# Kernel tuning notes

Measured on AMD Instinct MI355X. Metric: run time of the kernel, lower is better.

Reference implementation:

```python
import jax, jax.numpy as jnp
import numpy as np

RADIUS = 50.0
EPS = 1e-8


def setup_inputs() -> dict:
    key = jax.random.key(0)
    k1, k2, k3, k4, k5 = jax.random.split(key, 5)
    N, E, H = 16384, 524288, 256
    x = jax.random.normal(k1, (N, H), dtype=jnp.float32)
    edge_index = jax.random.randint(k2, (2, E), 0, N, dtype=jnp.int32)
    spatial_coords = jax.random.uniform(k3, (N, 2), dtype=jnp.float32) * 1000.0
    w1 = jax.random.normal(k4, (3, H // 2), dtype=jnp.float32) * 0.02
    b1 = jnp.zeros((H // 2,), dtype=jnp.float32)
    w2 = jax.random.normal(k5, (H // 2, H), dtype=jnp.float32) * 0.02
    b2 = jnp.zeros((H,), dtype=jnp.float32)
    return {"x": x, "edge_index": edge_index, "spatial_coords": spatial_coords,
            "w1": w1, "b1": b1, "w2": w2, "b2": b2}


def reference(x, edge_index, spatial_coords, w1, b1, w2, b2):
    N = x.shape[0]
    row, col = edge_index[0], edge_index[1]

    # degree via scatter-add (segment_sum)
    ones = jnp.ones(row.shape, dtype=x.dtype)
    degree = jax.ops.segment_sum(ones, row, num_segments=N)  # [N]

    # spatial density: count neighbors within RADIUS (full pairwise, vectorized)
    sq = jnp.sum(spatial_coords * spatial_coords, axis=-1)  # [N]
    d2 = sq[:, None] + sq[None, :] - 2.0 * (spatial_coords @ spatial_coords.T)  # [N,N] squared dists
    in_radius = (d2 <= RADIUS * RADIUS).astype(x.dtype)
    density = jnp.sum(in_radius, axis=1) - 1.0  # exclude self
    density = density / (jnp.max(density) + EPS)

    # local feature variance: || x - mean(neighbor features) ||
    nbr_sum = jax.ops.segment_sum(x[col], row, num_segments=N)  # [N,H]
    cnt = jnp.clip(degree, 1.0)[:, None]
    nbr_mean = nbr_sum / cnt
    fvar = jnp.linalg.norm(x - nbr_mean, axis=-1)  # [N]
    fvar = fvar / (jnp.max(fvar) + EPS)

    feats = jnp.stack([degree / (jnp.max(degree) + EPS), density, fvar], axis=-1)  # [N,3]
    h = jax.nn.relu(feats @ w1 + b1)
    return h @ w2 + b2  # [N, hidden_dim]
```

## Files before the change

### kernel.cpp

```cpp
#include <hip/hip_runtime.h>
#include <math.h>

#define R2 2500.0f
#define EPSF 1e-8f

constexpr int H  = 256;
constexpr int HH = 128;

__global__ void k_degree(const int* __restrict__ row, int* __restrict__ deg, int E) {
    int e = blockIdx.x * blockDim.x + threadIdx.x;
    if (e < E) atomicAdd(&deg[row[e]], 1);
}

__global__ void k_scan(const int* __restrict__ deg, int* __restrict__ row_ptr, int N) {
    __shared__ int s[1024];
    int t = threadIdx.x;
    int per = N >> 10;
    int base = t * per;
    int vals[32];
    int local = 0;
    for (int k = 0; k < per; k++) { vals[k] = deg[base + k]; local += vals[k]; }
    s[t] = local;
    __syncthreads();
    for (int off = 1; off < 1024; off <<= 1) {
        int v = s[t];
        int add = (t >= off) ? s[t - off] : 0;
        __syncthreads();
        s[t] = v + add;
        __syncthreads();
    }
    int excl = (t > 0) ? s[t - 1] : 0;
    for (int k = 0; k < per; k++) { row_ptr[base + k] = excl; excl += vals[k]; }
    if (t == 1023) row_ptr[N] = excl;
}

__global__ void k_fill(const int* __restrict__ row, const int* __restrict__ col,
                       const int* __restrict__ row_ptr, int* __restrict__ fill,
                       int* __restrict__ cols, int E) {
    int e = blockIdx.x * blockDim.x + threadIdx.x;
    if (e < E) {
        int r = row[e];
        int p = row_ptr[r] + atomicAdd(&fill[r], 1);
        cols[p] = col[e];
    }
}

__global__ void k_density(const float* __restrict__ coords, int* __restrict__ dens,
                          int N, int jPer) {
    __shared__ float sx[256], sy[256], sq[256];
    int i = blockIdx.x * 256 + threadIdx.x;
    const float2* c2 = (const float2*)coords;
    float2 ci = c2[i];
    float sqi = ci.x * ci.x + ci.y * ci.y;
    int j0 = blockIdx.y * jPer;
    int cnt = 0;
    for (int jt = j0; jt < j0 + jPer; jt += 256) {
        float2 cj = c2[jt + threadIdx.x];
        sx[threadIdx.x] = cj.x;
        sy[threadIdx.x] = cj.y;
        sq[threadIdx.x] = cj.x * cj.x + cj.y * cj.y;
        __syncthreads();
#pragma unroll 8
        for (int k = 0; k < 256; k++) {
            float dot = ci.x * sx[k] + ci.y * sy[k];
            float d2 = (sqi + sq[k]) - 2.0f * dot;
            cnt += (d2 <= R2) ? 1 : 0;
        }
        __syncthreads();
    }
    atomicAdd(&dens[i], cnt);
}

__global__ void __launch_bounds__(256) k_fvar(
    const float* __restrict__ x, const int* __restrict__ row_ptr,
    const int* __restrict__ cols, float* __restrict__ fvar, int N) {
    __shared__ float4 lds[4][8][64];
    int wave = threadIdx.x >> 6;
    int lane = threadIdx.x & 63;
    int i = blockIdx.x * 4 + wave;
    int s = row_ptr[i], e = row_ptr[i + 1];
    const float4* xb = (const float4*)x;
    float4 acc = make_float4(0.f, 0.f, 0.f, 0.f);
    for (int p0 = s; p0 < e; p0 += 64) {
        int m = e - p0; if (m > 64) m = 64;
        int idx = cols[p0 + (lane < m ? lane : m - 1)];
        for (int j = 0; j < m; j += 8) {
            int nb = m - j; if (nb > 8) nb = 8;
#pragma unroll
            for (int k = 0; k < 8; k++) {
                if (k < nb) {
                    int c = __shfl(idx, j + k, 64);
                    const float4* gp = xb + (size_t)c * 64 + lane;
                    __builtin_amdgcn_global_load_lds(
                        (const __attribute__((address_space(1))) void*)gp,
                        (__attribute__((address_space(3))) void*)(&lds[wave][k][0]),
                        16, 0, 0);
                }
            }
            __builtin_amdgcn_s_waitcnt(0);
#pragma unroll
            for (int k = 0; k < 8; k++) {
                if (k < nb) {
                    float4 v = lds[wave][k][lane];
                    acc.x += v.x; acc.y += v.y; acc.z += v.z; acc.w += v.w;
                }
            }
        }
    }
    float cnt = fmaxf((float)(e - s), 1.0f);
    float4 xi = xb[(size_t)i * 64 + lane];
    float dx = xi.x - acc.x / cnt;
    float dy = xi.y - acc.y / cnt;
    float dz = xi.z - acc.z / cnt;
    float dw = xi.w - acc.w / cnt;
    float ss = dx * dx + dy * dy + dz * dz + dw * dw;
#pragma unroll
    for (int off = 32; off > 0; off >>= 1) ss += __shfl_xor(ss, off, 64);
    if (lane == 0) fvar[i] = sqrtf(ss);
}

__global__ void __launch_bounds__(256) k_scal(
    const int* __restrict__ deg, const int* __restrict__ dens,
    const float* __restrict__ fvar, int* __restrict__ scal, int N) {
    __shared__ int sd[4], sn[4];
    __shared__ float sf[4];
    int t = threadIdx.x;
    int g = blockIdx.x * 256 + t;
    int stride = 256 * gridDim.x;
    int md = 0, mn = 0;
    float mf = 0.f;
    for (int i = g; i < N; i += stride) {
        md = max(md, deg[i]);
        mn = max(mn, dens[i]);
        mf = fmaxf(mf, fvar[i]);
    }
#pragma unroll
    for (int off = 32; off > 0; off >>= 1) {
        md = max(md, __shfl_xor(md, off, 64));
        mn = max(mn, __shfl_xor(mn, off, 64));
        mf = fmaxf(mf, __shfl_xor(mf, off, 64));
    }
    int w = t >> 6, l = t & 63;
    if (l == 0) { sd[w] = md; sn[w] = mn; sf[w] = mf; }
    __syncthreads();
    if (t == 0) {
#pragma unroll
        for (int k = 1; k < 4; k++) {
            md = max(md, sd[k]);
            mn = max(mn, sn[k]);
            mf = fmaxf(mf, sf[k]);
        }
        atomicMax(&scal[0], md);
        atomicMax(&scal[1], mn);
        atomicMax(&scal[2], __float_as_int(mf));
    }
}

__global__ void __launch_bounds__(256) k_mlp(
    const float* __restrict__ w1, const float* __restrict__ b1,
    const float* __restrict__ w2, const float* __restrict__ b2,
    const int* __restrict__ deg, const int* __restrict__ dens,
    const float* __restrict__ fvar, const int* __restrict__ scal,
    float* __restrict__ out, int N) {
    __shared__ float sh_h[HH];
    int j = threadIdx.x;
    float wv[HH];
#pragma unroll
    for (int l = 0; l < HH; l++) wv[l] = w2[l * H + j];
    float bj = b2[j];
    float maxdeg  = (float)scal[0] + EPSF;
    float maxdens = (float)(scal[1] - 1) + EPSF;
    float maxfv   = __int_as_float(scal[2]) + EPSF;
    float w1a = 0.f, w1b = 0.f, w1c = 0.f, b1j = 0.f;
    if (j < HH) { w1a = w1[j]; w1b = w1[HH + j]; w1c = w1[2 * HH + j]; b1j = b1[j]; }
    for (int i = blockIdx.x; i < N; i += gridDim.x) {
        float f0 = (float)deg[i] / maxdeg;
        float f1 = (float)(dens[i] - 1) / maxdens;
        float f2 = fvar[i] / maxfv;
        if (j < HH) {
            float h = f0 * w1a + f1 * w1b + f2 * w1c + b1j;
            sh_h[j] = fmaxf(h, 0.0f);
        }
        __syncthreads();
        float acc = bj;
#pragma unroll
        for (int l = 0; l < HH; l++) acc = fmaf(sh_h[l], wv[l], acc);
        out[(size_t)i * H + j] = acc;
        __syncthreads();
    }
}

extern "C" void kernel_launch(void* const* d_in, const int* in_sizes, int n_in,
                              void* d_out, int out_size, void* d_ws, size_t ws_size,
                              hipStream_t stream) {
    const float* x      = (const float*)d_in[0];
    const int*   ei     = (const int*)d_in[1];
    const float* coords = (const float*)d_in[2];
    const float* w1     = (const float*)d_in[3];
    const float* b1     = (const float*)d_in[4];
    const float* w2     = (const float*)d_in[5];
    const float* b2     = (const float*)d_in[6];
    float* out = (float*)d_out;

    const int N = in_sizes[2] / 2;
    const int E = in_sizes[1] / 2;
    const int* row = ei;
    const int* col = ei + E;

    int* ws       = (int*)d_ws;
    int* deg_cnt  = ws;
    int* dens_cnt = ws + N;
    int* fill     = ws + 2 * N;
    int* scal     = ws + 3 * N;
    float* fvarp  = (float*)(ws + 3 * N + 4);
    int* row_ptr  = ws + 4 * N + 4;
    int* cols     = ws + 5 * N + 5;

    hipMemsetAsync(ws, 0, (size_t)(3 * N + 4) * sizeof(int), stream);

    int eb = (E + 255) / 256;
    k_degree<<<eb, 256, 0, stream>>>(row, deg_cnt, E);
    k_scan<<<1, 1024, 0, stream>>>(deg_cnt, row_ptr, N);
    k_fill<<<eb, 256, 0, stream>>>(row, col, row_ptr, fill, cols, E);

    const int NSLICE = 8;
    k_density<<<dim3(N / 256, NSLICE), 256, 0, stream>>>(coords, dens_cnt, N, N / NSLICE);

    k_fvar<<<N / 4, 256, 0, stream>>>(x, row_ptr, cols, fvarp, N);

    k_scal<<<64, 256, 0, stream>>>(deg_cnt, dens_cnt, fvarp, scal, N);

    k_mlp<<<1024, 256, 0, stream>>>(w1, b1, w2, b2, deg_cnt, dens_cnt, fvarp, scal,
                                    out, N);
}
```

Baseline: 297.4 us.

## Double-buffer neighbor gather in fvar and precompute packed coords for density

The fvar kernel now double-buffers its LDS gather: the next batch of eight neighbor rows is issued before the current batch is consumed, using a partial vmcnt wait so loads overlap accumulation. Its blocks shrink to two waves. A new prep kernel packs x, y and squared norm into a float4 per point, so the density kernel reads uniform global float4 loads in place of staging through shared memory with barriers. The density j-range is also split into 16 slices instead of 8. The risks are the hand-written waitcnt logic, clamped duplicate loads for partial batches, and an extra kernel launch.

```diff
diff --git a/kernel.cpp b/kernel.cpp
--- a/kernel.cpp
+++ b/kernel.cpp
@@ -45,63 +45,74 @@
     }
 }
 
-__global__ void k_density(const float* __restrict__ coords, int* __restrict__ dens,
-                          int N, int jPer) {
-    __shared__ float sx[256], sy[256], sq[256];
+__global__ void k_prep(const float* __restrict__ coords, float4* __restrict__ pj, int N) {
+    int i = blockIdx.x * 256 + threadIdx.x;
+    if (i < N) {
+        float2 c = ((const float2*)coords)[i];
+        pj[i] = make_float4(c.x, c.y, c.x * c.x + c.y * c.y, 0.0f);
+    }
+}
+
+__global__ void __launch_bounds__(256) k_density(
+    const float* __restrict__ coords, const float4* __restrict__ pj,
+    int* __restrict__ dens, int N, int jPer) {
     int i = blockIdx.x * 256 + threadIdx.x;
     const float2* c2 = (const float2*)coords;
     float2 ci = c2[i];
     float sqi = ci.x * ci.x + ci.y * ci.y;
     int j0 = blockIdx.y * jPer;
     int cnt = 0;
-    for (int jt = j0; jt < j0 + jPer; jt += 256) {
-        float2 cj = c2[jt + threadIdx.x];
-        sx[threadIdx.x] = cj.x;
-        sy[threadIdx.x] = cj.y;
-        sq[threadIdx.x] = cj.x * cj.x + cj.y * cj.y;
-        __syncthreads();
 #pragma unroll 8
-        for (int k = 0; k < 256; k++) {
-            float dot = ci.x * sx[k] + ci.y * sy[k];
-            float d2 = (sqi + sq[k]) - 2.0f * dot;
-            cnt += (d2 <= R2) ? 1 : 0;
-        }
-        __syncthreads();
+    for (int j = j0; j < j0 + jPer; j++) {
+        float4 q = pj[j];
+        float dot = ci.x * q.x + ci.y * q.y;
+        float d2 = (sqi + q.z) - 2.0f * dot;
+        cnt += (d2 <= R2) ? 1 : 0;
     }
     atomicAdd(&dens[i], cnt);
 }
 
-__global__ void __launch_bounds__(256) k_fvar(
+__global__ void __launch_bounds__(128) k_fvar(
     const float* __restrict__ x, const int* __restrict__ row_ptr,
     const int* __restrict__ cols, float* __restrict__ fvar, int N) {
-    __shared__ float4 lds[4][8][64];
+    __shared__ float4 lds[2][2][8][64];
     int wave = threadIdx.x >> 6;
     int lane = threadIdx.x & 63;
-    int i = blockIdx.x * 4 + wave;
+    int i = blockIdx.x * 2 + wave;
     int s = row_ptr[i], e = row_ptr[i + 1];
     const float4* xb = (const float4*)x;
     float4 acc = make_float4(0.f, 0.f, 0.f, 0.f);
     for (int p0 = s; p0 < e; p0 += 64) {
         int m = e - p0; if (m > 64) m = 64;
         int idx = cols[p0 + (lane < m ? lane : m - 1)];
-        for (int j = 0; j < m; j += 8) {
-            int nb = m - j; if (nb > 8) nb = 8;
+        int nbat = (m + 7) >> 3;
+        auto issue = [&](int b, int buf) {
+#pragma unroll
+            for (int k = 0; k < 8; k++) {
+                int sl = 8 * b + k; if (sl > m - 1) sl = m - 1;
+                int c = __shfl(idx, sl, 64);
+                const float4* gp = xb + (size_t)c * 64 + lane;
+                __builtin_amdgcn_global_load_lds(
+                    (const __attribute__((address_space(1))) void*)gp,
+                    (__attribute__((address_space(3))) void*)(&lds[wave][buf][k][0]),
+                    16, 0, 0);
+            }
+        };
+        issue(0, 0);
+        for (int b = 0; b < nbat; b++) {
+            if (b + 1 < nbat) {
+                asm volatile("s_waitcnt lgkmcnt(0)" ::: "memory");
+                issue(b + 1, (b + 1) & 1);
+                asm volatile("s_waitcnt vmcnt(8)" ::: "memory");
+            } else {
+                asm volatile("s_waitcnt vmcnt(0)" ::: "memory");
+            }
+            __builtin_amdgcn_sched_barrier(0);
+            int nb = m - 8 * b; if (nb > 8) nb = 8;
 #pragma unroll
             for (int k = 0; k < 8; k++) {
                 if (k < nb) {
-                    int c = __shfl(idx, j + k, 64);
-                    const float4* gp = xb + (size_t)c * 64 + lane;
-                    __builtin_amdgcn_global_load_lds(
-                        (const __attribute__((address_space(1))) void*)gp,
-                        (__attribute__((address_space(3))) void*)(&lds[wave][k][0]),
-                        16, 0, 0);
-                }
-            }
-            __builtin_amdgcn_s_waitcnt(0);
-#pragma unroll
-            for (int k = 0; k < 8; k++) {
-                if (k < nb) {
-                    float4 v = lds[wave][k][lane];
+                    float4 v = lds[wave][b & 1][k][lane];
                     acc.x += v.x; acc.y += v.y; acc.z += v.z; acc.w += v.w;
                 }
             }
@@ -215,6 +226,7 @@
     float* fvarp  = (float*)(ws + 3 * N + 4);
     int* row_ptr  = ws + 4 * N + 4;
     int* cols     = ws + 5 * N + 5;
+    float4* pj    = (float4*)(ws + ((5 * N + 5 + E + 3) & ~3));
 
     hipMemsetAsync(ws, 0, (size_t)(3 * N + 4) * sizeof(int), stream);
 
@@ -223,10 +235,11 @@
     k_scan<<<1, 1024, 0, stream>>>(deg_cnt, row_ptr, N);
     k_fill<<<eb, 256, 0, stream>>>(row, col, row_ptr, fill, cols, E);
 
-    const int NSLICE = 8;
-    k_density<<<dim3(N / 256, NSLICE), 256, 0, stream>>>(coords, dens_cnt, N, N / NSLICE);
-
-    k_fvar<<<N / 4, 256, 0, stream>>>(x, row_ptr, cols, fvarp, N);
+    k_prep<<<N / 256, 256, 0, stream>>>(coords, pj, N);
+    const int NSLICE = 16;
+    k_density<<<dim3(N / 256, NSLICE), 256, 0, stream>>>(coords, pj, dens_cnt, N, N / NSLICE);
+
+    k_fvar<<<N / 2, 128, 0, stream>>>(x, row_ptr, cols, fvarp, N);
 
     k_scal<<<64, 256, 0, stream>>>(deg_cnt, dens_cnt, fvarp, scal, N);
 
```

Measured after the change: 305.9 us. 2.9% more time.
